# Performance work log

Measured on AMD Instinct MI355X. Metric: run time of the kernel, lower is better.

Reference implementation:

```python
import jax, jax.numpy as jnp
import numpy as np

H = 32  # LSTM hidden size (hardcoded in module)
N = 2 * H  # attention feature dim = 64


def setup_inputs() -> dict:
    key = jax.random.key(0)
    ks = jax.random.split(key, 16)
    B, T = 4096, 512
    inp = {
        "y_t_1_embed": jax.random.normal(ks[0], (B, 1), jnp.float32),
        "h0": jax.random.normal(ks[1], (1, B, H), jnp.float32),
        "c0": jax.random.normal(ks[2], (1, B, H), jnp.float32),
        "encoder_outputs": jax.random.normal(ks[3], (B, T, N), jnp.float32),
        "encoder_feature": jax.random.normal(ks[4], (B * T, N), jnp.float32),
        # LSTM params (PyTorch layout: gates ordered i, f, g, o)
        "W_ih": jax.random.normal(ks[5], (4 * H, 1), jnp.float32) * 0.1,
        "W_hh": jax.random.normal(ks[6], (4 * H, H), jnp.float32) * 0.1,
        "b_ih": jax.random.normal(ks[7], (4 * H,), jnp.float32) * 0.1,
        "b_hh": jax.random.normal(ks[8], (4 * H,), jnp.float32) * 0.1,
        # attention params
        "W_proj": jax.random.normal(ks[9], (N, N), jnp.float32) * 0.1,
        "b_proj": jax.random.normal(ks[10], (N,), jnp.float32) * 0.1,
        "v_w": jax.random.normal(ks[11], (N,), jnp.float32) * 0.1,
        # output MLP params
        "W1": jax.random.normal(ks[12], (N, 2 * N), jnp.float32) * 0.1,
        "b1": jax.random.normal(ks[13], (N,), jnp.float32) * 0.1,
        "W2": jax.random.normal(ks[14], (1, N), jnp.float32) * 0.1,
        "b2": jax.random.normal(ks[15], (1,), jnp.float32) * 0.1,
    }
    return inp


def _decoder_fwd(y, h0, c0, enc_out, enc_feat,
                 W_ih, W_hh, b_ih, b_hh, W_proj, b_proj, v_w, W1, b1, W2, b2):
    B, T, n = enc_out.shape
    h, c = h0[0], c0[0]  # [B, H]
    # single LSTM step (seq_len == 1)
    gates = y @ W_ih.T + h @ W_hh.T + (b_ih + b_hh)  # [B, 4H]
    i, f, g, o = jnp.split(gates, 4, axis=-1)
    c_new = jax.nn.sigmoid(f) * c + jax.nn.sigmoid(i) * jnp.tanh(g)
    h_new = jax.nn.sigmoid(o) * jnp.tanh(c_new)
    s_t_hat = jnp.concatenate([h_new, c_new], axis=1)  # [B, 2H]
    # additive (Bahdanau) attention
    dec_fea = s_t_hat @ W_proj.T + b_proj  # [B, N]
    e = jnp.tanh(enc_feat.reshape(B, T, n) + dec_fea[:, None, :])  # [B, T, N]
    scores = jnp.einsum("btn,n->bt", e, v_w)
    attn = jax.nn.softmax(scores, axis=-1)  # [B, T]
    c_t = jnp.einsum("bt,btn->bn", attn, enc_out)  # [B, N]
    # output MLP
    out_in = jnp.concatenate([s_t_hat, c_t], axis=1)  # [B, 2N]
    output = (out_in @ W1.T + b1) @ W2.T + b2  # [B, 1]
    return output, h_new[None], c_new[None]


def reference(y_t_1_embed, h0, c0, encoder_outputs, encoder_feature,
              W_ih, W_hh, b_ih, b_hh, W_proj, b_proj, v_w, W1, b1, W2, b2):
    return _decoder_fwd(y_t_1_embed, h0, c0, encoder_outputs, encoder_feature,
                        W_ih, W_hh, b_ih, b_hh, W_proj, b_proj, v_w, W1, b1, W2, b2)
```

## Files before the change

kernel.cpp:

```cpp
#include <hip/hip_runtime.h>

#define HH 32
#define NN 64
#define TMAX 512

__device__ __forceinline__ float ftanh(float x) {
    float a = __builtin_amdgcn_exp2f(x * 2.885390082f);
    float r = __builtin_amdgcn_rcpf(a + 1.0f);
    return __builtin_fmaf(-2.0f, r, 1.0f);
}
__device__ __forceinline__ float fsigmoid(float x) {
    float a = __builtin_amdgcn_exp2f(x * -1.442695041f);
    return __builtin_amdgcn_rcpf(1.0f + a);
}
__device__ __forceinline__ float fexp(float x) {
    return __builtin_amdgcn_exp2f(x * 1.442695041f);
}

__global__ __launch_bounds__(256) void decoder_fused(
    const float* __restrict__ y, const float* __restrict__ h0, const float* __restrict__ c0,
    const float* __restrict__ enc_out, const float* __restrict__ enc_feat,
    const float* __restrict__ W_ih, const float* __restrict__ W_hh,
    const float* __restrict__ b_ih, const float* __restrict__ b_hh,
    const float* __restrict__ W_proj, const float* __restrict__ b_proj,
    const float* __restrict__ v_w,
    const float* __restrict__ W1, const float* __restrict__ b1,
    const float* __restrict__ W2, const float* __restrict__ b2,
    float* __restrict__ out, int B, int T)
{
    const int b   = blockIdx.x;
    const int tid = threadIdx.x;

    __shared__ float s_h[HH];
    __shared__ float s_cstate[HH];
    __shared__ float s_gates[4 * HH];
    __shared__ float s_outin[2 * NN];
    __shared__ float s_decfea[NN];
    __shared__ float s_vw[NN];
    __shared__ float s_e[TMAX];
    __shared__ float s_ct[16 * NN];
    __shared__ float s_l[16];

    if (tid < HH) {
        s_h[tid]      = h0[(size_t)b * HH + tid];
        s_cstate[tid] = c0[(size_t)b * HH + tid];
    }
    if (tid >= 64 && tid < 128) s_vw[tid - 64] = v_w[tid - 64];
    __syncthreads();

    if (tid < 4 * HH) {
        float acc = y[b] * W_ih[tid] + b_ih[tid] + b_hh[tid];
        const float* wr = W_hh + tid * HH;
        #pragma unroll
        for (int k = 0; k < HH; ++k) acc += wr[k] * s_h[k];
        s_gates[tid] = acc;
    }
    __syncthreads();

    if (tid < HH) {
        float ig = fsigmoid(s_gates[tid]);
        float fg = fsigmoid(s_gates[HH + tid]);
        float gg = ftanh(s_gates[2 * HH + tid]);
        float og = fsigmoid(s_gates[3 * HH + tid]);
        float cn = fg * s_cstate[tid] + ig * gg;
        float hn = og * ftanh(cn);
        s_outin[tid]      = hn;
        s_outin[HH + tid] = cn;
        out[(size_t)B + (size_t)b * HH + tid]                  = hn;
        out[(size_t)B + (size_t)B * HH + (size_t)b * HH + tid] = cn;
    }
    __syncthreads();

    if (tid < NN) {
        float acc = b_proj[tid];
        const float* wr = W_proj + tid * NN;
        #pragma unroll
        for (int k = 0; k < NN; ++k) acc += wr[k] * s_outin[k];
        s_decfea[tid] = acc;
    }
    __syncthreads();

    const int tg = tid >> 4;
    const int nc = tid & 15;
    const int n0 = nc * 4;
    const float4* ef = (const float4*)(enc_feat + (size_t)b * T * NN);
    const float4* eo = (const float4*)(enc_out  + (size_t)b * T * NN);
    const float vw0 = s_vw[n0], vw1 = s_vw[n0 + 1], vw2 = s_vw[n0 + 2], vw3 = s_vw[n0 + 3];
    const float df0 = s_decfea[n0], df1 = s_decfea[n0 + 1], df2 = s_decfea[n0 + 2], df3 = s_decfea[n0 + 3];

    float lsum = 0.0f;
    #pragma unroll 4
    for (int t0 = 0; t0 < T; t0 += 16) {
        const int t = t0 + tg;
        float4 u = ef[t * 16 + nc];
        float p = vw0 * ftanh(u.x + df0) + vw1 * ftanh(u.y + df1)
                + vw2 * ftanh(u.z + df2) + vw3 * ftanh(u.w + df3);
        p += __shfl_xor(p, 1);
        p += __shfl_xor(p, 2);
        p += __shfl_xor(p, 4);
        p += __shfl_xor(p, 8);
        float e = fexp(p);
        lsum += e;
        if (nc == 0) s_e[t] = e;
    }
    if (nc == 0) s_l[tg] = lsum;

    float ax = 0.f, ay = 0.f, az = 0.f, aw = 0.f;
    #pragma unroll 4
    for (int t0 = 0; t0 < T; t0 += 16) {
        const int t = t0 + tg;
        float e = s_e[t];
        float4 v = eo[t * 16 + nc];
        ax += e * v.x; ay += e * v.y; az += e * v.z; aw += e * v.w;
    }
    s_ct[tg * NN + n0]     = ax;
    s_ct[tg * NN + n0 + 1] = ay;
    s_ct[tg * NN + n0 + 2] = az;
    s_ct[tg * NN + n0 + 3] = aw;
    __syncthreads();

    if (tid < NN) {
        float num = 0.0f, L = 0.0f;
        #pragma unroll
        for (int g = 0; g < 16; ++g) { num += s_ct[g * NN + tid]; L += s_l[g]; }
        s_outin[NN + tid] = num / L;
    }
    __syncthreads();

    float v2 = 0.0f;
    if (tid < NN) {
        float acc = b1[tid];
        const float* wr = W1 + tid * 2 * NN;
        #pragma unroll
        for (int k = 0; k < 2 * NN; ++k) acc += wr[k] * s_outin[k];
        v2 = acc * W2[tid];
    }
    if (tid < 64) {
        #pragma unroll
        for (int mask = 32; mask >= 1; mask >>= 1) v2 += __shfl_xor(v2, mask);
        if (tid == 0) out[b] = v2 + b2[0];
    }
}

extern "C" void kernel_launch(void* const* d_in, const int* in_sizes, int n_in,
                              void* d_out, int out_size, void* d_ws, size_t ws_size,
                              hipStream_t stream) {
    const float* y        = (const float*)d_in[0];
    const float* h0       = (const float*)d_in[1];
    const float* c0       = (const float*)d_in[2];
    const float* enc_out  = (const float*)d_in[3];
    const float* enc_feat = (const float*)d_in[4];
    const float* W_ih     = (const float*)d_in[5];
    const float* W_hh     = (const float*)d_in[6];
    const float* b_ih     = (const float*)d_in[7];
    const float* b_hh     = (const float*)d_in[8];
    const float* W_proj   = (const float*)d_in[9];
    const float* b_proj   = (const float*)d_in[10];
    const float* v_w      = (const float*)d_in[11];
    const float* W1       = (const float*)d_in[12];
    const float* b1       = (const float*)d_in[13];
    const float* W2       = (const float*)d_in[14];
    const float* b2       = (const float*)d_in[15];
    float* out = (float*)d_out;

    const int B = in_sizes[0];
    const int T = in_sizes[3] / (B * NN);

    decoder_fused<<<B, 256, 0, stream>>>(
        y, h0, c0, enc_out, enc_feat, W_ih, W_hh, b_ih, b_hh,
        W_proj, b_proj, v_w, W1, b1, W2, b2, out, B, T);
}
```

Before: 205.8 us.

## Prefetch encoder tiles before LSTM prologue and software-pipeline attention loops

Issues the first 64 timesteps of enc_feat and enc_out loads into registers at kernel start, so they overlap the serial LSTM and projection prologue. Both attention loops are software-pipelined: the next chunk is loaded while the current one is processed. Shuffle reductions become DPP row reductions, and __syncthreads becomes a barrier that waits only on LDS counters, so outstanding global loads stay in flight across barriers. The cost is higher register pressure (eight float4 buffers per thread) and an assumption that T is a multiple of 64.

```diff
diff --git a/kernel.cpp b/kernel.cpp
--- a/kernel.cpp
+++ b/kernel.cpp
@@ -3,6 +3,9 @@
 #define HH 32
 #define NN 64
 #define TMAX 512
+
+#define BAR() do { asm volatile("s_waitcnt lgkmcnt(0)" ::: "memory"); \
+                   __builtin_amdgcn_s_barrier(); } while (0)
 
 __device__ __forceinline__ float ftanh(float x) {
     float a = __builtin_amdgcn_exp2f(x * 2.885390082f);
@@ -15,6 +18,14 @@
 }
 __device__ __forceinline__ float fexp(float x) {
     return __builtin_amdgcn_exp2f(x * 1.442695041f);
+}
+__device__ __forceinline__ float rowsum16(float x) {
+    int t;
+    t = __builtin_amdgcn_update_dpp(0, __float_as_int(x), 0x128, 0xF, 0xF, true); x += __int_as_float(t);
+    t = __builtin_amdgcn_update_dpp(0, __float_as_int(x), 0x124, 0xF, 0xF, true); x += __int_as_float(t);
+    t = __builtin_amdgcn_update_dpp(0, __float_as_int(x), 0x122, 0xF, 0xF, true); x += __int_as_float(t);
+    t = __builtin_amdgcn_update_dpp(0, __float_as_int(x), 0x121, 0xF, 0xF, true); x += __int_as_float(t);
+    return x;
 }
 
 __global__ __launch_bounds__(256) void decoder_fused(
@@ -30,6 +41,9 @@
 {
     const int b   = blockIdx.x;
     const int tid = threadIdx.x;
+    const int tg  = tid >> 4;
+    const int nc  = tid & 15;
+    const int n0  = nc * 4;
 
     __shared__ float s_h[HH];
     __shared__ float s_cstate[HH];
@@ -41,12 +55,24 @@
     __shared__ float s_ct[16 * NN];
     __shared__ float s_l[16];
 
+    const float4* ef = (const float4*)(enc_feat + (size_t)b * T * NN);
+    const float4* eo = (const float4*)(enc_out  + (size_t)b * T * NN);
+
+    float4 fb0 = ef[(  0 + tg) * 16 + nc];
+    float4 fb1 = ef[( 16 + tg) * 16 + nc];
+    float4 fb2 = ef[( 32 + tg) * 16 + nc];
+    float4 fb3 = ef[( 48 + tg) * 16 + nc];
+    float4 ob0 = eo[(  0 + tg) * 16 + nc];
+    float4 ob1 = eo[( 16 + tg) * 16 + nc];
+    float4 ob2 = eo[( 32 + tg) * 16 + nc];
+    float4 ob3 = eo[( 48 + tg) * 16 + nc];
+
     if (tid < HH) {
         s_h[tid]      = h0[(size_t)b * HH + tid];
         s_cstate[tid] = c0[(size_t)b * HH + tid];
     }
     if (tid >= 64 && tid < 128) s_vw[tid - 64] = v_w[tid - 64];
-    __syncthreads();
+    BAR();
 
     if (tid < 4 * HH) {
         float acc = y[b] * W_ih[tid] + b_ih[tid] + b_hh[tid];
@@ -55,7 +81,7 @@
         for (int k = 0; k < HH; ++k) acc += wr[k] * s_h[k];
         s_gates[tid] = acc;
     }
-    __syncthreads();
+    BAR();
 
     if (tid < HH) {
         float ig = fsigmoid(s_gates[tid]);
@@ -69,7 +95,7 @@
         out[(size_t)B + (size_t)b * HH + tid]                  = hn;
         out[(size_t)B + (size_t)B * HH + (size_t)b * HH + tid] = cn;
     }
-    __syncthreads();
+    BAR();
 
     if (tid < NN) {
         float acc = b_proj[tid];
@@ -78,46 +104,65 @@
         for (int k = 0; k < NN; ++k) acc += wr[k] * s_outin[k];
         s_decfea[tid] = acc;
     }
-    __syncthreads();
-
-    const int tg = tid >> 4;
-    const int nc = tid & 15;
-    const int n0 = nc * 4;
-    const float4* ef = (const float4*)(enc_feat + (size_t)b * T * NN);
-    const float4* eo = (const float4*)(enc_out  + (size_t)b * T * NN);
+    BAR();
+
     const float vw0 = s_vw[n0], vw1 = s_vw[n0 + 1], vw2 = s_vw[n0 + 2], vw3 = s_vw[n0 + 3];
     const float df0 = s_decfea[n0], df1 = s_decfea[n0 + 1], df2 = s_decfea[n0 + 2], df3 = s_decfea[n0 + 3];
 
+    #define PROCB(U, T_) do { \
+        float p = vw0 * ftanh((U).x + df0) + vw1 * ftanh((U).y + df1) \
+                + vw2 * ftanh((U).z + df2) + vw3 * ftanh((U).w + df3); \
+        p = rowsum16(p); \
+        float e = fexp(p); \
+        lsum += e; \
+        if (nc == 0) s_e[T_] = e; \
+    } while (0)
+
+    const int CMAX = T >> 6;
     float lsum = 0.0f;
-    #pragma unroll 4
-    for (int t0 = 0; t0 < T; t0 += 16) {
-        const int t = t0 + tg;
-        float4 u = ef[t * 16 + nc];
-        float p = vw0 * ftanh(u.x + df0) + vw1 * ftanh(u.y + df1)
-                + vw2 * ftanh(u.z + df2) + vw3 * ftanh(u.w + df3);
-        p += __shfl_xor(p, 1);
-        p += __shfl_xor(p, 2);
-        p += __shfl_xor(p, 4);
-        p += __shfl_xor(p, 8);
-        float e = fexp(p);
-        lsum += e;
-        if (nc == 0) s_e[t] = e;
+    #pragma unroll 1
+    for (int c = 0; c < CMAX - 1; ++c) {
+        const int t0 = c * 64;
+        { float4 u = fb0; fb0 = ef[(t0 +  64 + tg) * 16 + nc]; PROCB(u, t0 +      tg); }
+        { float4 u = fb1; fb1 = ef[(t0 +  80 + tg) * 16 + nc]; PROCB(u, t0 + 16 + tg); }
+        { float4 u = fb2; fb2 = ef[(t0 +  96 + tg) * 16 + nc]; PROCB(u, t0 + 32 + tg); }
+        { float4 u = fb3; fb3 = ef[(t0 + 112 + tg) * 16 + nc]; PROCB(u, t0 + 48 + tg); }
+    }
+    {
+        const int t0 = (CMAX - 1) * 64;
+        PROCB(fb0, t0 +      tg);
+        PROCB(fb1, t0 + 16 + tg);
+        PROCB(fb2, t0 + 32 + tg);
+        PROCB(fb3, t0 + 48 + tg);
     }
     if (nc == 0) s_l[tg] = lsum;
 
+    #define PROCC(V, T_) do { \
+        float e = s_e[T_]; \
+        ax += e * (V).x; ay += e * (V).y; az += e * (V).z; aw += e * (V).w; \
+    } while (0)
+
     float ax = 0.f, ay = 0.f, az = 0.f, aw = 0.f;
-    #pragma unroll 4
-    for (int t0 = 0; t0 < T; t0 += 16) {
-        const int t = t0 + tg;
-        float e = s_e[t];
-        float4 v = eo[t * 16 + nc];
-        ax += e * v.x; ay += e * v.y; az += e * v.z; aw += e * v.w;
+    #pragma unroll 1
+    for (int c = 0; c < CMAX - 1; ++c) {
+        const int t0 = c * 64;
+        { float4 v = ob0; ob0 = eo[(t0 +  64 + tg) * 16 + nc]; PROCC(v, t0 +      tg); }
+        { float4 v = ob1; ob1 = eo[(t0 +  80 + tg) * 16 + nc]; PROCC(v, t0 + 16 + tg); }
+        { float4 v = ob2; ob2 = eo[(t0 +  96 + tg) * 16 + nc]; PROCC(v, t0 + 32 + tg); }
+        { float4 v = ob3; ob3 = eo[(t0 + 112 + tg) * 16 + nc]; PROCC(v, t0 + 48 + tg); }
+    }
+    {
+        const int t0 = (CMAX - 1) * 64;
+        PROCC(ob0, t0 +      tg);
+        PROCC(ob1, t0 + 16 + tg);
+        PROCC(ob2, t0 + 32 + tg);
+        PROCC(ob3, t0 + 48 + tg);
     }
     s_ct[tg * NN + n0]     = ax;
     s_ct[tg * NN + n0 + 1] = ay;
     s_ct[tg * NN + n0 + 2] = az;
     s_ct[tg * NN + n0 + 3] = aw;
-    __syncthreads();
+    BAR();
 
     if (tid < NN) {
         float num = 0.0f, L = 0.0f;
@@ -125,7 +170,7 @@
         for (int g = 0; g < 16; ++g) { num += s_ct[g * NN + tid]; L += s_l[g]; }
         s_outin[NN + tid] = num / L;
     }
-    __syncthreads();
+    BAR();
 
     float v2 = 0.0f;
     if (tid < NN) {
```

Measured after the change: 192.2 us (median of 2 runs). -6.6%, faster.
